# Kernel tuning notes

Measured on AMD Instinct MI355X. Metric: run time of the kernel, lower is better.

The kernel has to match this reference:

```python
import jax, jax.numpy as jnp
import numpy as np

N_NODES = 100000
N_EDGES = 3200000
N_GRAPHS = 1000


def gcn_conv(x, row, col, norm, W, b, num_nodes):
    # x: [N, F_in] -> [N, F_out]; PyG GCNConv: linear, then normalized scatter-add
    h = x @ W                                   # [N, F_out]
    msg = norm[:, None] * h[row]                # gather from source nodes
    out = jax.ops.segment_sum(msg, col, num_segments=num_nodes)  # scatter to targets
    return out + b


def gcn_norm(edge_index, edge_weight, num_nodes):
    # add self-loops with weight 1.0 (PyG default, improved=False)
    loops = jnp.arange(num_nodes, dtype=edge_index.dtype)
    row = jnp.concatenate([edge_index[0], loops])
    col = jnp.concatenate([edge_index[1], loops])
    w = jnp.concatenate([edge_weight, jnp.ones(num_nodes, edge_weight.dtype)])
    deg = jax.ops.segment_sum(w, col, num_segments=num_nodes)
    dinv = jnp.where(deg > 0, jax.lax.rsqrt(jnp.maximum(deg, 1e-30)), 0.0)
    norm = dinv[row] * w * dinv[col]
    return row, col, norm


def setup_inputs() -> dict:
    key = jax.random.key(0)
    ks = jax.random.split(key, 8)
    x = jax.random.normal(ks[0], (N_NODES, 3), dtype=jnp.float32)
    edge_index = jax.random.randint(ks[1], (2, N_EDGES), 0, N_NODES, dtype=jnp.int64)
    edge_weight = jax.random.uniform(ks[2], (N_EDGES,), dtype=jnp.float32)
    batch = jnp.sort(jax.random.randint(ks[3], (N_NODES,), 0, N_GRAPHS, dtype=jnp.int64))
    W1 = jax.random.normal(ks[4], (3, 16), dtype=jnp.float32) * (1.0 / np.sqrt(3))
    b1 = jnp.zeros((16,), jnp.float32)
    W2 = jax.random.normal(ks[5], (16, 16), dtype=jnp.float32) * 0.25
    b2 = jnp.zeros((16,), jnp.float32)
    Wlin = jax.random.normal(ks[6], (16, 7), dtype=jnp.float32) * 0.25
    blin = jnp.zeros((7,), jnp.float32)
    return {"x": x, "edge_index": edge_index, "edge_weight": edge_weight,
            "batch": batch, "W1": W1, "b1": b1, "W2": W2, "b2": b2,
            "Wlin": Wlin, "blin": blin}


def reference(x, edge_index, edge_weight, batch, W1, b1, W2, b2, Wlin, blin):
    num_nodes = x.shape[0]
    row, col, norm = gcn_norm(edge_index, edge_weight, num_nodes)
    h = jax.nn.relu(gcn_conv(x, row, col, norm, W1, b1, num_nodes))
    h = jax.nn.relu(gcn_conv(h, row, col, norm, W2, b2, num_nodes))
    pooled = jax.ops.segment_sum(h, batch, num_segments=N_GRAPHS)  # [G, 16]
    return pooled @ Wlin + blin  # [G, 7]
```

## Files before the change

### kernel.cpp

```cpp
#include <hip/hip_runtime.h>


#define SH 6
#define RB 64
#define KMAX 2048
#define KST (KMAX + 1)
#define TPB 256
#define BCAP 4096
#define PT 1024
#define PB 256
#define NP 4
#define ETCAP 12800
#define GSPAN 16

typedef unsigned short ushort_t;
typedef unsigned char u8;
typedef unsigned long long u64;

__device__ __forceinline__ ushort_t f2bf(float v) {
    unsigned u = __float_as_uint(v);
    u += 0x7FFFu + ((u >> 16) & 1u);
    return (ushort_t)(u >> 16);
}

__device__ __forceinline__ unsigned quantw(float w) {
    unsigned wq = (unsigned)__float2int_rn(w * 32768.0f);
    return wq > 32767u ? 32767u : wq;
}

__global__ __launch_bounds__(PT)
void k_part(const int* __restrict__ row, const int* __restrict__ col,
            const float* __restrict__ ew, unsigned* __restrict__ bcnt,
            unsigned* __restrict__ done, unsigned* __restrict__ bst,
            unsigned* __restrict__ bof, uint2* __restrict__ brc,
            int E, int K, int tile, int KP) {
    __shared__ unsigned lh[KMAX];
    __shared__ unsigned cur[KMAX];
    __shared__ unsigned wt[PT / 64];
    __shared__ unsigned lastFlag;
    __shared__ unsigned lc[ETCAP];
    __shared__ unsigned lp[ETCAP];
    int tid = threadIdx.x, b = blockIdx.x;
    int e0 = min(b * tile, E), e1 = min(b * tile + tile, E);
    int cnt = e1 - e0;
    unsigned base = (unsigned)e0;
    bool staged = (cnt <= ETCAP);
    for (int i = tid; i < KMAX; i += PT) lh[i] = 0u;
    __syncthreads();
    if (staged) {
        for (int j = tid; j < cnt; j += PT) {
            int e = e0 + j;
            int c = col[e];
            lc[j] = (unsigned)c;
            lp[j] = (unsigned)row[e] | (quantw(ew[e]) << 17);
            atomicAdd(&lh[c >> SH], 1u);
        }
    } else {
        for (int e = e0 + tid; e < e1; e += PT) atomicAdd(&lh[col[e] >> SH], 1u);
    }
    __syncthreads();
    for (int i = tid; i < K; i += PT) {
        unsigned c = lh[i];
        if (c) atomicAdd(&bcnt[i], c);
    }
    __syncthreads();
    if (tid == 0) {
        __threadfence();
        lastFlag = (atomicAdd(done, 1u) == (unsigned)(gridDim.x - 1)) ? 1u : 0u;
    }
    __syncthreads();
    if (lastFlag) {
        int i0g = tid << 1;
        unsigned g0 = (i0g < K) ? atomicAdd(&bcnt[i0g], 0u) : 0u;
        unsigned g1 = (i0g + 1 < K) ? atomicAdd(&bcnt[i0g + 1], 0u) : 0u;
        unsigned ts = g0 + g1, v = ts;
#pragma unroll
        for (int o = 1; o < 64; o <<= 1) {
            unsigned u = __shfl_up(v, o, 64);
            if ((tid & 63) >= o) v += u;
        }
        if ((tid & 63) == 63) wt[tid >> 6] = v;
        __syncthreads();
        if (tid == 0) {
            unsigned acc = 0;
#pragma unroll
            for (int w = 0; w < PT / 64; w++) { unsigned t = wt[w]; wt[w] = acc; acc += t; }
        }
        __syncthreads();
        unsigned ex = wt[tid >> 6] + (v - ts);
        if (i0g < K) bst[i0g] = ex;
        if (i0g + 1 < K) bst[i0g + 1] = ex + g0;
        __syncthreads();
    }
    int i0 = tid << 1;
    unsigned a0 = lh[i0], a1 = lh[i0 + 1];
    unsigned ts = a0 + a1, v = ts;
#pragma unroll
    for (int o = 1; o < 64; o <<= 1) {
        unsigned u = __shfl_up(v, o, 64);
        if ((tid & 63) >= o) v += u;
    }
    if ((tid & 63) == 63) wt[tid >> 6] = v;
    __syncthreads();
    if (tid == 0) {
        unsigned acc = 0;
#pragma unroll
        for (int w = 0; w < PT / 64; w++) { unsigned t = wt[w]; wt[w] = acc; acc += t; }
    }
    __syncthreads();
    unsigned ex = wt[tid >> 6] + (v - ts);
    unsigned* bo = bof + (size_t)b * KST;
    cur[i0] = base + ex;          bo[i0] = base + ex;
    cur[i0 + 1] = base + ex + a0; bo[i0 + 1] = base + ex + a0;
    if (tid == PT - 1) bo[KMAX] = base + ex + ts;
    __syncthreads();
    for (int p = 0; p < NP; ++p) {
        int lo = p * KP, hi = min(lo + KP, K);
        if (staged) {
            for (int j = tid; j < cnt; j += PT) {
                unsigned c = lc[j];
                int bkt = (int)(c >> SH);
                if (bkt >= lo && bkt < hi) {
                    unsigned pos = atomicAdd(&cur[bkt], 1u);
                    brc[pos] = make_uint2(lp[j], c);
                }
            }
        } else {
            for (int e = e0 + tid; e < e1; e += PT) {
                int c = col[e];
                int bkt = c >> SH;
                if (bkt >= lo && bkt < hi) {
                    unsigned pos = atomicAdd(&cur[bkt], 1u);
                    brc[pos] = make_uint2((unsigned)row[e] | (quantw(ew[e]) << 17),
                                          (unsigned)c);
                }
            }
        }
        __syncthreads();
    }
}

__global__ __launch_bounds__(TPB)
void k_grp(const uint2* __restrict__ brc, const unsigned* __restrict__ bof,
           const unsigned* __restrict__ bst, const float* __restrict__ x,
           const float* __restrict__ W1, unsigned* __restrict__ srt,
           unsigned* __restrict__ cptr, float* __restrict__ dinv,
           unsigned* __restrict__ g1b, int N, int E, int K) {
    int orig = blockIdx.x;
    int q8 = K >> 3, r8 = K & 7;
    int xcd = orig & 7, idx = orig >> 3;
    int k = (xcd < r8 ? xcd * (q8 + 1) : r8 * (q8 + 1) + (xcd - r8) * q8) + idx;
    int node0 = k << SH;

    __shared__ unsigned ebuf[BCAP];
    __shared__ u8 cbuf[BCAP];
    __shared__ u8 seg[BCAP];
    __shared__ unsigned rsrc[PB];
    __shared__ unsigned roff[PB + 1];
    __shared__ unsigned wt4[TPB / 64];
    __shared__ unsigned cnt64[RB], st64[RB], dq[RB];
    __shared__ float dl[RB], lx[RB * 3], lw[48];
    int tid = threadIdx.x;
    unsigned s = bst[k];
    if (tid < RB) { cnt64[tid] = 0u; dq[tid] = 0u; }
    if (tid < 48) lw[tid] = W1[tid];
    int nn = min(RB, N - node0);
    for (int i = tid; i < nn * 3; i += TPB) lx[i] = x[(size_t)node0 * 3 + i];

    unsigned rl;
    {
        unsigned s0 = bof[(size_t)tid * KST + k];
        unsigned s1 = bof[(size_t)tid * KST + k + 1];
        rsrc[tid] = s0;
        rl = s1 - s0;
    }
    unsigned v = rl;
#pragma unroll
    for (int o = 1; o < 64; o <<= 1) {
        unsigned u = __shfl_up(v, o, 64);
        if ((tid & 63) >= o) v += u;
    }
    if ((tid & 63) == 63) wt4[tid >> 6] = v;
    __syncthreads();
    if (tid == 0) {
        unsigned acc = 0;
#pragma unroll
        for (int w = 0; w < TPB / 64; w++) { unsigned t = wt4[w]; wt4[w] = acc; acc += t; }
    }
    __syncthreads();
    unsigned ex = wt4[tid >> 6] + (v - rl);
    roff[tid] = ex;
    if (tid == PB - 1) roff[PB] = ex + rl;
    __syncthreads();
    unsigned c = roff[PB];

    bool fits = (c <= (unsigned)BCAP);
    if (fits) {
        for (unsigned j = ex; j < ex + rl; ++j) seg[j] = (u8)tid;
        __syncthreads();
        for (unsigned j = tid; j < c; j += TPB) {
            unsigned r = seg[j];
            unsigned src = rsrc[r] + (j - roff[r]);
            uint2 p = brc[src];
            unsigned cl = p.y & 63u;
            ebuf[j] = p.x; cbuf[j] = (u8)cl;
            atomicAdd(&cnt64[cl], 1u);
            atomicAdd(&dq[cl], p.x >> 17);
        }
        __syncthreads();
        if (tid == 0) {
            unsigned acc = 0;
            for (int i = 0; i < RB; i++) { st64[i] = acc; acc += cnt64[i]; cnt64[i] = 0u; }
        }
        __syncthreads();
        for (unsigned j = tid; j < c; j += TPB) {
            unsigned cl = cbuf[j];
            unsigned pos = st64[cl] + atomicAdd(&cnt64[cl], 1u);
            srt[s + pos] = ebuf[j];
        }
    } else {
#define MAP_SRC(j, srcv)                                                       \
        {                                                                      \
            int lo = 0, hi = PB - 1;                                           \
            _Pragma("unroll")                                                  \
            for (int it = 0; it < 8; ++it) {                                   \
                int mid = (lo + hi + 1) >> 1;                                  \
                if (roff[mid] <= (j)) lo = mid; else hi = mid - 1;             \
            }                                                                  \
            (srcv) = rsrc[lo] + ((j) - roff[lo]);                              \
        }
        for (unsigned j = tid; j < c; j += TPB) {
            unsigned src; MAP_SRC(j, src);
            uint2 p = brc[src];
            unsigned cl = p.y & 63u;
            atomicAdd(&cnt64[cl], 1u);
            atomicAdd(&dq[cl], p.x >> 17);
        }
        __syncthreads();
        if (tid == 0) {
            unsigned acc = 0;
            for (int i = 0; i < RB; i++) { st64[i] = acc; acc += cnt64[i]; cnt64[i] = 0u; }
        }
        __syncthreads();
        for (unsigned j = tid; j < c; j += TPB) {
            unsigned src; MAP_SRC(j, src);
            uint2 p = brc[src];
            unsigned cl = p.y & 63u;
            unsigned pos = st64[cl] + atomicAdd(&cnt64[cl], 1u);
            srt[s + pos] = p.x;
        }
#undef MAP_SRC
    }
    __syncthreads();
    if (tid < RB) {
        float d = rsqrtf(1.0f + (float)dq[tid] * (1.0f / 32768.0f));
        dl[tid] = d;
        if (tid < nn) {
            dinv[node0 + tid] = d;
            cptr[node0 + tid] = s + st64[tid];
        }
    }
    if (tid == 0 && node0 + nn == N) cptr[N] = (unsigned)E;
    __syncthreads();
    float* gtmp = (float*)ebuf;
    for (int idx2 = tid; idx2 < nn * 16; idx2 += TPB) {
        int n = idx2 >> 4, f = idx2 & 15;
        float vv = dl[n] * (lx[n * 3] * lw[f] + lx[n * 3 + 1] * lw[16 + f] +
                            lx[n * 3 + 2] * lw[32 + f]);
        gtmp[idx2] = vv;
    }
    __syncthreads();
    for (int idx2 = tid; idx2 < nn * 8; idx2 += TPB) {
        int n = idx2 >> 3, qq = idx2 & 7;
        g1b[(size_t)(node0 + n) * 8 + qq] =
            (unsigned)f2bf(gtmp[n * 16 + 2 * qq]) |
            ((unsigned)f2bf(gtmp[n * 16 + 2 * qq + 1]) << 16);
    }
}

__global__ __launch_bounds__(TPB)
void k_csr1(const unsigned* __restrict__ srt, const unsigned* __restrict__ cptr,
            const uint2* __restrict__ gb2, const float* __restrict__ x,
            const float* __restrict__ W1, const float* __restrict__ dinv,
            const float* __restrict__ b1, const float* __restrict__ W2,
            unsigned* __restrict__ g2b, float* __restrict__ acc2, int N) {
    int t = blockIdx.x * TPB + threadIdx.x;
    int c = t >> 2, f4 = t & 3;
    if (c >= N) return;
    unsigned e = cptr[c], end = cptr[c + 1];
    float s0 = 0.0f, s1 = 0.0f, s2 = 0.0f, s3 = 0.0f;
#pragma unroll 4
    for (; e < end; ++e) {
        unsigned m = srt[e];
        float w = (float)(m >> 17) * (1.0f / 32768.0f);
        uint2 u = gb2[(size_t)(m & 0x1FFFFu) * 4 + f4];
        s0 = fmaf(w, __uint_as_float(u.x << 16), s0);
        s1 = fmaf(w, __uint_as_float(u.x & 0xFFFF0000u), s1);
        s2 = fmaf(w, __uint_as_float(u.y << 16), s2);
        s3 = fmaf(w, __uint_as_float(u.y & 0xFFFF0000u), s3);
    }
    float d = dinv[c];
    float xx0 = x[(size_t)c * 3], xx1 = x[(size_t)c * 3 + 1], xx2 = x[(size_t)c * 3 + 2];
    const float4 w0 = *(const float4*)&W1[4 * f4];
    const float4 w1 = *(const float4*)&W1[16 + 4 * f4];
    const float4 w2 = *(const float4*)&W1[32 + 4 * f4];
    float g0 = d * (xx0 * w0.x + xx1 * w1.x + xx2 * w2.x);
    float g1 = d * (xx0 * w0.y + xx1 * w1.y + xx2 * w2.y);
    float g2 = d * (xx0 * w0.z + xx1 * w1.z + xx2 * w2.z);
    float g3 = d * (xx0 * w0.w + xx1 * w1.w + xx2 * w2.w);
    const float4 bb = *(const float4*)&b1[4 * f4];
    float h[4];
    h[0] = fmaxf(bb.x + d * (g0 + s0), 0.0f);
    h[1] = fmaxf(bb.y + d * (g1 + s1), 0.0f);
    h[2] = fmaxf(bb.z + d * (g2 + s2), 0.0f);
    h[3] = fmaxf(bb.w + d * (g3 + s3), 0.0f);
    int base = (threadIdx.x & 63) & ~3;
    float o0 = 0.0f, o1 = 0.0f, o2 = 0.0f, o3 = 0.0f;
#pragma unroll
    for (int kk = 0; kk < 16; ++kk) {
        float hk = __shfl(h[kk & 3], base + (kk >> 2), 64);
        const float4 wv = *(const float4*)&W2[kk * 16 + 4 * f4];
        o0 = fmaf(hk, wv.x, o0);
        o1 = fmaf(hk, wv.y, o1);
        o2 = fmaf(hk, wv.z, o2);
        o3 = fmaf(hk, wv.w, o3);
    }
    float r0 = d * o0, r1 = d * o1, r2 = d * o2, r3 = d * o3;
    *(float4*)&acc2[(size_t)c * 16 + 4 * f4] = make_float4(r0, r1, r2, r3);
    g2b[(size_t)c * 8 + 2 * f4]     = (unsigned)f2bf(r0) | ((unsigned)f2bf(r1) << 16);
    g2b[(size_t)c * 8 + 2 * f4 + 1] = (unsigned)f2bf(r2) | ((unsigned)f2bf(r3) << 16);
}

__global__ __launch_bounds__(TPB)
void k_csr2(const unsigned* __restrict__ srt, const unsigned* __restrict__ cptr,
            const uint2* __restrict__ gb2, const float* __restrict__ acc2,
            const float* __restrict__ dinv, const float* __restrict__ b2,
            const int* __restrict__ batch, float* __restrict__ pooled,
            int N, int G) {
    __shared__ float lacc[GSPAN * 16];
    __shared__ int lb[64];
    int tid = threadIdx.x;
    int t = blockIdx.x * TPB + tid;
    int c = t >> 2, f4 = t & 3;
    int c0 = blockIdx.x * 64;
    int ncols = min(64, N - c0);
    if (tid < ncols) lb[tid] = batch[c0 + tid];
    if (tid < GSPAN * 16) lacc[tid] = 0.0f;
    __syncthreads();
    int gmin = lb[0], gmax = lb[ncols - 1];
    bool fits = (gmax - gmin) < GSPAN;

    if (c < N) {
        unsigned e = cptr[c], end = cptr[c + 1];
        float s0 = 0.0f, s1 = 0.0f, s2 = 0.0f, s3 = 0.0f;
#pragma unroll 4
        for (; e < end; ++e) {
            unsigned m = srt[e];
            float w = (float)(m >> 17) * (1.0f / 32768.0f);
            uint2 u = gb2[(size_t)(m & 0x1FFFFu) * 4 + f4];
            s0 = fmaf(w, __uint_as_float(u.x << 16), s0);
            s1 = fmaf(w, __uint_as_float(u.x & 0xFFFF0000u), s1);
            s2 = fmaf(w, __uint_as_float(u.y << 16), s2);
            s3 = fmaf(w, __uint_as_float(u.y & 0xFFFF0000u), s3);
        }
        float d = dinv[c];
        const float4 se = *(const float4*)&acc2[(size_t)c * 16 + 4 * f4];
        const float4 bb = *(const float4*)&b2[4 * f4];
        float h0 = fmaxf(bb.x + d * (se.x + s0), 0.0f);
        float h1 = fmaxf(bb.y + d * (se.y + s1), 0.0f);
        float h2 = fmaxf(bb.z + d * (se.z + s2), 0.0f);
        float h3 = fmaxf(bb.w + d * (se.w + s3), 0.0f);
        int g = lb[c - c0];
        if (fits) {
            int o = (g - gmin) * 16 + 4 * f4;
            atomicAdd(&lacc[o],     h0);
            atomicAdd(&lacc[o + 1], h1);
            atomicAdd(&lacc[o + 2], h2);
            atomicAdd(&lacc[o + 3], h3);
        } else {
            atomicAdd(&pooled[(size_t)g * 16 + 4 * f4],     h0);
            atomicAdd(&pooled[(size_t)g * 16 + 4 * f4 + 1], h1);
            atomicAdd(&pooled[(size_t)g * 16 + 4 * f4 + 2], h2);
            atomicAdd(&pooled[(size_t)g * 16 + 4 * f4 + 3], h3);
        }
    }
    if (fits) {
        __syncthreads();
        if (tid < GSPAN * 16) {
            int g = gmin + (tid >> 4);
            float v = lacc[tid];
            if (g < G && v != 0.0f) atomicAdd(&pooled[(size_t)g * 16 + (tid & 15)], v);
        }
    }
}

__global__ void k_final(const float* __restrict__ pooled, const float* __restrict__ Wlin,
                        const float* __restrict__ blin, float* __restrict__ out, int G) {
    int t = blockIdx.x * blockDim.x + threadIdx.x;
    int g = t / 7, j = t % 7;
    if (g >= G) return;
    float v = blin[j];
#pragma unroll
    for (int f = 0; f < 16; f++) v += pooled[g * 16 + f] * Wlin[f * 7 + j];
    out[g * 7 + j] = v;
}

static inline int cdiv_i(long long a, long long b) { return (int)((a + b - 1) / b); }

extern "C" void kernel_launch(void* const* d_in, const int* in_sizes, int n_in,
                              void* d_out, int out_size, void* d_ws, size_t ws_size,
                              hipStream_t stream) {
    const float* x     = (const float*)d_in[0];
    const int*   ei    = (const int*)d_in[1];
    const float* ew    = (const float*)d_in[2];
    const int*   batch = (const int*)d_in[3];
    const float* W1    = (const float*)d_in[4];
    const float* b1    = (const float*)d_in[5];
    const float* W2    = (const float*)d_in[6];
    const float* b2    = (const float*)d_in[7];
    const float* Wlin  = (const float*)d_in[8];
    const float* blin  = (const float*)d_in[9];
    float* out = (float*)d_out;

    const int N = in_sizes[0] / 3;
    const int E = in_sizes[2];
    const int G = out_size / 7;
    const int K = (N + RB - 1) >> SH;
    const int tile = cdiv_i(E, PB);
    const int KP = cdiv_i(K, NP);
    const int* row = ei;
    const int* col = ei + E;

    uint2*    brc    = (uint2*)d_ws;
    unsigned* srt    = (unsigned*)(brc + E);
    float*    dinv   = (float*)(srt + E);
    unsigned* g1b    = (unsigned*)(dinv + N);
    unsigned* g2b    = g1b + (size_t)N * 8;
    float*    acc2   = (float*)(g2b + (size_t)N * 8);
    unsigned* cptr   = (unsigned*)(acc2 + (size_t)N * 16);
    unsigned* bst    = cptr + N + 1;
    unsigned* bof    = bst + KMAX;
    unsigned* bcnt   = bof + (size_t)PB * KST;
    unsigned* done   = bcnt + KMAX;
    float*    pooled = (float*)(done + 1);

    hipMemsetAsync(bcnt, 0, (KMAX + 1 + (size_t)G * 16) * sizeof(unsigned), stream);

    k_part<<<PB, PT, 0, stream>>>(row, col, ew, bcnt, done, bst, bof, brc,
                                  E, K, tile, KP);
    k_grp<<<K, TPB, 0, stream>>>(brc, bof, bst, x, W1, srt, cptr, dinv, g1b,
                                 N, E, K);

    k_csr1<<<cdiv_i((long long)N * 4, TPB), TPB, 0, stream>>>(
        srt, cptr, (const uint2*)g1b, x, W1, dinv, b1, W2, g2b, acc2, N);

    k_csr2<<<cdiv_i((long long)N * 4, TPB), TPB, 0, stream>>>(
        srt, cptr, (const uint2*)g2b, acc2, dinv, b2, batch, pooled, N, G);

    k_final<<<cdiv_i((long long)G * 7, TPB), TPB, 0, stream>>>(pooled, Wlin, blin, out, G);
}
```

Baseline: 216.7 us.

## Replace LDS-staged segment gather in k_grp with per-thread run loops

The k_grp grouping kernel no longer computes a block-wide prefix over the per-partition runs or stages edges in LDS buffers with a segment map. Each thread now walks its own contiguous run from bof directly, once to count and once to scatter, reading brc from global memory both times. This removes the scan, most barriers and the large shared buffers, which should raise occupancy. In exchange, edges are read twice from global memory, and per-thread serial loops over uneven run lengths give worse load balance and less coalesced access across a wavefront.

```diff
diff --git a/kernel.cpp b/kernel.cpp
--- a/kernel.cpp
+++ b/kernel.cpp
@@ -6,7 +6,6 @@
 #define KMAX 2048
 #define KST (KMAX + 1)
 #define TPB 256
-#define BCAP 4096
 #define PT 1024
 #define PB 256
 #define NP 4
@@ -152,14 +151,9 @@
     int k = (xcd < r8 ? xcd * (q8 + 1) : r8 * (q8 + 1) + (xcd - r8) * q8) + idx;
     int node0 = k << SH;
 
-    __shared__ unsigned ebuf[BCAP];
-    __shared__ u8 cbuf[BCAP];
-    __shared__ u8 seg[BCAP];
-    __shared__ unsigned rsrc[PB];
-    __shared__ unsigned roff[PB + 1];
-    __shared__ unsigned wt4[TPB / 64];
     __shared__ unsigned cnt64[RB], st64[RB], dq[RB];
     __shared__ float dl[RB], lx[RB * 3], lw[48];
+    __shared__ float gtmp[RB * 16];
     int tid = threadIdx.x;
     unsigned s = bst[k];
     if (tid < RB) { cnt64[tid] = 0u; dq[tid] = 0u; }
@@ -167,89 +161,27 @@
     int nn = min(RB, N - node0);
     for (int i = tid; i < nn * 3; i += TPB) lx[i] = x[(size_t)node0 * 3 + i];
 
-    unsigned rl;
-    {
-        unsigned s0 = bof[(size_t)tid * KST + k];
-        unsigned s1 = bof[(size_t)tid * KST + k + 1];
-        rsrc[tid] = s0;
-        rl = s1 - s0;
-    }
-    unsigned v = rl;
-#pragma unroll
-    for (int o = 1; o < 64; o <<= 1) {
-        unsigned u = __shfl_up(v, o, 64);
-        if ((tid & 63) >= o) v += u;
-    }
-    if ((tid & 63) == 63) wt4[tid >> 6] = v;
+    unsigned s0 = bof[(size_t)tid * KST + k];
+    unsigned s1 = bof[(size_t)tid * KST + k + 1];
+    __syncthreads();
+
+    for (unsigned j = s0; j < s1; ++j) {
+        uint2 p = brc[j];
+        unsigned cl = p.y & 63u;
+        atomicAdd(&cnt64[cl], 1u);
+        atomicAdd(&dq[cl], p.x >> 17);
+    }
     __syncthreads();
     if (tid == 0) {
         unsigned acc = 0;
-#pragma unroll
-        for (int w = 0; w < TPB / 64; w++) { unsigned t = wt4[w]; wt4[w] = acc; acc += t; }
-    }
-    __syncthreads();
-    unsigned ex = wt4[tid >> 6] + (v - rl);
-    roff[tid] = ex;
-    if (tid == PB - 1) roff[PB] = ex + rl;
-    __syncthreads();
-    unsigned c = roff[PB];
-
-    bool fits = (c <= (unsigned)BCAP);
-    if (fits) {
-        for (unsigned j = ex; j < ex + rl; ++j) seg[j] = (u8)tid;
-        __syncthreads();
-        for (unsigned j = tid; j < c; j += TPB) {
-            unsigned r = seg[j];
-            unsigned src = rsrc[r] + (j - roff[r]);
-            uint2 p = brc[src];
-            unsigned cl = p.y & 63u;
-            ebuf[j] = p.x; cbuf[j] = (u8)cl;
-            atomicAdd(&cnt64[cl], 1u);
-            atomicAdd(&dq[cl], p.x >> 17);
-        }
-        __syncthreads();
-        if (tid == 0) {
-            unsigned acc = 0;
-            for (int i = 0; i < RB; i++) { st64[i] = acc; acc += cnt64[i]; cnt64[i] = 0u; }
-        }
-        __syncthreads();
-        for (unsigned j = tid; j < c; j += TPB) {
-            unsigned cl = cbuf[j];
-            unsigned pos = st64[cl] + atomicAdd(&cnt64[cl], 1u);
-            srt[s + pos] = ebuf[j];
-        }
-    } else {
-#define MAP_SRC(j, srcv)                                                       \
-        {                                                                      \
-            int lo = 0, hi = PB - 1;                                           \
-            _Pragma("unroll")                                                  \
-            for (int it = 0; it < 8; ++it) {                                   \
-                int mid = (lo + hi + 1) >> 1;                                  \
-                if (roff[mid] <= (j)) lo = mid; else hi = mid - 1;             \
-            }                                                                  \
-            (srcv) = rsrc[lo] + ((j) - roff[lo]);                              \
-        }
-        for (unsigned j = tid; j < c; j += TPB) {
-            unsigned src; MAP_SRC(j, src);
-            uint2 p = brc[src];
-            unsigned cl = p.y & 63u;
-            atomicAdd(&cnt64[cl], 1u);
-            atomicAdd(&dq[cl], p.x >> 17);
-        }
-        __syncthreads();
-        if (tid == 0) {
-            unsigned acc = 0;
-            for (int i = 0; i < RB; i++) { st64[i] = acc; acc += cnt64[i]; cnt64[i] = 0u; }
-        }
-        __syncthreads();
-        for (unsigned j = tid; j < c; j += TPB) {
-            unsigned src; MAP_SRC(j, src);
-            uint2 p = brc[src];
-            unsigned cl = p.y & 63u;
-            unsigned pos = st64[cl] + atomicAdd(&cnt64[cl], 1u);
-            srt[s + pos] = p.x;
-        }
-#undef MAP_SRC
+        for (int i = 0; i < RB; i++) { st64[i] = acc; acc += cnt64[i]; cnt64[i] = 0u; }
+    }
+    __syncthreads();
+    for (unsigned j = s0; j < s1; ++j) {
+        uint2 p = brc[j];
+        unsigned cl = p.y & 63u;
+        unsigned pos = st64[cl] + atomicAdd(&cnt64[cl], 1u);
+        srt[s + pos] = p.x;
     }
     __syncthreads();
     if (tid < RB) {
@@ -262,7 +194,6 @@
     }
     if (tid == 0 && node0 + nn == N) cptr[N] = (unsigned)E;
     __syncthreads();
-    float* gtmp = (float*)ebuf;
     for (int idx2 = tid; idx2 < nn * 16; idx2 += TPB) {
         int n = idx2 >> 4, f = idx2 & 15;
         float vv = dl[n] * (lx[n * 3] * lw[f] + lx[n * 3 + 1] * lw[16 + f] +
```

Result: slower. 247.0 us (+14.0%).
